# Optimization experiments

Hardware: AMD Instinct MI355X
Metric: run time of the kernel (lower is better)

Reference implementation:

```python
import jax, jax.numpy as jnp
import numpy as np

N = 50000      # nodes
E = 800000     # edges (avg degree 16)
LM = 1024      # lm_dim
H = 128        # hidden_channels
OUT = 64       # out_channels


def setup_inputs() -> dict:
    key = jax.random.key(0)
    ks = jax.random.split(key, 13)
    s = 0.02
    return {
        "x": jax.random.normal(ks[0], (N,), dtype=jnp.float32),
        "x_out": jax.random.normal(ks[1], (N, LM), dtype=jnp.float32),
        "c": jax.random.normal(ks[2], (N,), dtype=jnp.float32),
        "edge_index": jax.random.randint(ks[3], (2, E), 0, N, dtype=jnp.int64),
        "edge_weight": jax.random.uniform(ks[4], (E,), dtype=jnp.float32),
        # weights stored as [in, out]
        "Wa": jax.random.normal(ks[5], (1, LM), dtype=jnp.float32) * s,   # aa_linear (no bias)
        "Wc": jax.random.normal(ks[6], (1, LM), dtype=jnp.float32) * s,   # c_linear (no bias)
        "Wl": jax.random.normal(ks[7], (LM, LM), dtype=jnp.float32) * s,  # lm_linear
        "bl": jax.random.normal(ks[8], (LM,), dtype=jnp.float32) * s,
        "W1": jax.random.normal(ks[9], (LM, H), dtype=jnp.float32) * s,   # conv1
        "b1": jax.random.normal(ks[10], (H,), dtype=jnp.float32) * s,
        "W3": jax.random.normal(ks[11], (H, OUT), dtype=jnp.float32) * s,  # conv3
        "b3": jax.random.normal(ks[12], (OUT,), dtype=jnp.float32) * s,
    }


def gcn_conv(h, src, dst, ew, W, b, n):
    """PyG GCNConv with normalize=True, add_self_loops=True."""
    h = h @ W                                   # [n, out]
    loop = jnp.arange(n, dtype=src.dtype)
    src_f = jnp.concatenate([src, loop])
    dst_f = jnp.concatenate([dst, loop])
    ew_f = jnp.concatenate([ew, jnp.ones((n,), ew.dtype)])
    deg = jax.ops.segment_sum(ew_f, dst_f, num_segments=n)     # in-degree incl. self-loops
    dis = jnp.where(deg > 0, jax.lax.rsqrt(deg), 0.0)          # deg^{-1/2}
    norm = dis[src_f] * ew_f * dis[dst_f]                      # per-edge coefficient
    out = jax.ops.segment_sum(norm[:, None] * h[src_f], dst_f, num_segments=n)
    return out + b


def reference(x, x_out, c, edge_index, edge_weight, Wa, Wc, Wl, bl, W1, b1, W3, b3):
    # (c_linear(c[:,None]) + aa_linear(x[:,None]) + lm_linear(x_out)).relu()
    h = jax.nn.relu(c[:, None] * Wc[0] + x[:, None] * Wa[0] + x_out @ Wl + bl)  # [N, LM]
    src, dst = edge_index[0], edge_index[1]
    h = jax.nn.relu(gcn_conv(h, src, dst, edge_weight, W1, b1, N))              # [N, H]
    return gcn_conv(h, src, dst, edge_weight, W3, b3, N)                        # [N, OUT]
```

## Files before the change

### kernel.cpp

```cpp
#include <hip/hip_runtime.h>
#include <hip/hip_bf16.h>

typedef unsigned short u16;
typedef __attribute__((ext_vector_type(8))) short bf16x8;
typedef __attribute__((ext_vector_type(4))) float f32x4;

constexpr int NN = 50000;
constexpr int NE = 800000;
constexpr int LM = 1024;
constexpr int HC = 128;
constexpr int OC = 64;

constexpr size_t OFF_ROWPTR = 0;
constexpr size_t OFF_CURSOR = 200192;
constexpr size_t OFF_COUNTS = 400384;
constexpr size_t OFF_INCL   = 600576;
constexpr size_t OFF_BSUM   = 800768;
constexpr size_t OFF_BOFF   = 801024;
constexpr size_t OFF_DIS    = 801280;
constexpr size_t OFF_CSRC   = 1001472;
constexpr size_t OFF_CSW    = 4201472;
constexpr size_t OFF_WLT    = 7401472;
constexpr size_t OFF_W1T    = 9498624;
constexpr size_t OFF_H      = 9760768;
constexpr size_t OFF_Y1     = 112160768;
constexpr size_t OFF_H1     = 124960768;
constexpr size_t OFF_Y3     = 137760768;

__device__ __forceinline__ u16 f2bf(float f) {
    union { float f; unsigned int u; } a; a.f = f;
    unsigned int u = a.u + 0x7FFFu + ((a.u >> 16) & 1u);
    return (u16)(u >> 16);
}
__device__ __forceinline__ float bf2f(u16 v) {
    union { unsigned int u; float f; } a; a.u = ((unsigned int)v) << 16;
    return a.f;
}
__device__ __forceinline__ ushort2 pkbf(float a, float b) {
    union { __hip_bfloat162 h; ushort2 u; } cv;
    cv.h = __float22bfloat162_rn(make_float2(a, b));
    return cv.u;
}
__device__ __forceinline__ void async_copy16(u16* lds, const u16* g) {
    __builtin_amdgcn_global_load_lds(
        (const __attribute__((address_space(1))) void*)g,
        (__attribute__((address_space(3))) void*)lds, 16, 0, 0);
}

__global__ void k_zero(int* counts) {
    int i = blockIdx.x * 256 + threadIdx.x;
    if (i < NN) counts[i] = 0;
}
__global__ void k_count(const int* __restrict__ ei, int* __restrict__ counts) {
    int e = blockIdx.x * 256 + threadIdx.x;
    if (e < NE) atomicAdd(&counts[ei[NE + e]], 1);
}
__global__ void k_scan1(const int* __restrict__ counts, int* __restrict__ incl,
                        int* __restrict__ bsum) {
    __shared__ int sm[1024];
    int t = threadIdx.x, idx = blockIdx.x * 1024 + t;
    int v = (idx < NN) ? counts[idx] : 0;
    sm[t] = v; __syncthreads();
    for (int off = 1; off < 1024; off <<= 1) {
        int add = (t >= off) ? sm[t - off] : 0;
        __syncthreads();
        sm[t] += add;
        __syncthreads();
    }
    if (idx < NN) incl[idx] = sm[t];
    if (t == 1023) bsum[blockIdx.x] = sm[t];
}
__global__ void k_scan2(const int* __restrict__ bsum, int* __restrict__ boff, int nb) {
    if (threadIdx.x == 0 && blockIdx.x == 0) {
        int run = 0;
        for (int i = 0; i < nb; i++) { boff[i] = run; run += bsum[i]; }
    }
}
__global__ void k_scan3(const int* __restrict__ incl, const int* __restrict__ counts,
                        const int* __restrict__ boff, int* __restrict__ rowptr,
                        int* __restrict__ cursor) {
    int idx = blockIdx.x * 256 + threadIdx.x;
    if (idx < NN) {
        int rp = incl[idx] - counts[idx] + boff[idx >> 10];
        rowptr[idx] = rp;
        cursor[idx] = rp;
    } else if (idx == NN) {
        rowptr[NN] = NE;
    }
}
__global__ void k_fill(const int* __restrict__ ei, const float* __restrict__ ew,
                       int* __restrict__ cursor, int* __restrict__ csrc,
                       float* __restrict__ csw) {
    int e = blockIdx.x * 256 + threadIdx.x;
    if (e < NE) {
        int d = ei[NE + e];
        int slot = atomicAdd(&cursor[d], 1);
        csrc[slot] = ei[e];
        csw[slot] = ew[e];
    }
}
__global__ void k_deg(const int* __restrict__ rowptr, const float* __restrict__ csw,
                      float* __restrict__ dis) {
    int i = blockIdx.x * 256 + threadIdx.x;
    if (i >= NN) return;
    float d = 1.0f;
    int p1 = rowptr[i + 1];
    for (int p = rowptr[i]; p < p1; ++p) d += csw[p];
    dis[i] = rsqrtf(d);
}
__global__ void k_wnorm(const int* __restrict__ csrc, float* __restrict__ csw,
                        const float* __restrict__ dis) {
    int p = blockIdx.x * 256 + threadIdx.x;
    if (p < NE) csw[p] = csw[p] * dis[csrc[p]];
}

__global__ void k_cvtWl(const float* __restrict__ Wl, u16* __restrict__ WlT) {
    __shared__ float sm[32][33];
    int k0 = blockIdx.y * 32, n0 = blockIdx.x * 32;
    sm[threadIdx.y][threadIdx.x] = Wl[(size_t)(k0 + threadIdx.y) * LM + n0 + threadIdx.x];
    __syncthreads();
    WlT[(size_t)(n0 + threadIdx.y) * LM + k0 + threadIdx.x] = f2bf(sm[threadIdx.x][threadIdx.y]);
}
__global__ void k_cvtW1(const float* __restrict__ W1, u16* __restrict__ W1T) {
    int idx = blockIdx.x * 256 + threadIdx.x;
    if (idx >= HC * LM) return;
    int o = idx >> 10, k = idx & 1023;
    W1T[idx] = f2bf(W1[(size_t)k * HC + o]);
}

template <int MODE>
__global__ __launch_bounds__(256, 2) void k_gemm(
    const void* __restrict__ Aptr, const u16* __restrict__ Bt, u16* __restrict__ Cout,
    int M, int Nn, int K, int nby,
    const float* __restrict__ xv, const float* __restrict__ cv,
    const float* __restrict__ Wa, const float* __restrict__ Wc,
    const float* __restrict__ bl) {
    __shared__ u16 lA[128 * 64];
    __shared__ u16 lB[128 * 64];
    const int tid = threadIdx.x;
    const int lane = tid & 63, wv = tid >> 6;
    const int mtiles = (M + 127) >> 7;
    int bx, by;
    if (nby > 1) {
        int x = blockIdx.x & 7, j = blockIdx.x >> 3;
        bx = (j & ~7) | x;
        by = j & 7;
        if (bx >= mtiles) return;
    } else {
        bx = blockIdx.x; by = 0;
    }
    const int m0 = bx * 128, n0 = by * 128;
    const int wm = (wv >> 1) * 64, wn = (wv & 1) * 64;
    const int fr = lane & 15, qd = lane >> 4;
    const int nt = K >> 6;

    f32x4 acc[4][4] = {};
    const float* A32 = (const float*)Aptr;

    int srl[4], sslot[4]; const float* sbase[4];
    float4 pf[8];
    if constexpr (MODE == 1) {
        #pragma unroll
        for (int i = 0; i < 4; i++) {
            int cidx = i * 256 + tid;
            srl[i] = cidx >> 3; sslot[i] = cidx & 7;
            int k8 = sslot[i] ^ (srl[i] & 7);
            int row = m0 + srl[i]; if (row >= M) row = M - 1;
            sbase[i] = A32 + (size_t)row * K + k8 * 8;
        }
        #pragma unroll
        for (int i = 0; i < 4; i++) {
            pf[2 * i]     = *(const float4*)(sbase[i]);
            pf[2 * i + 1] = *(const float4*)(sbase[i] + 4);
        }
    }

    for (int kt = 0; kt < nt; kt++) {
        const int k0 = kt << 6;
        __syncthreads();
        #pragma unroll
        for (int i = 0; i < 4; i++) {
            int r0 = i * 32 + wv * 8;
            int rl = r0 + (lane >> 3);
            int slot = lane & 7;
            int k8 = slot ^ (rl & 7);
            int col = n0 + rl; if (col >= Nn) col = Nn - 1;
            const u16* g = Bt + (size_t)col * K + k0 + k8 * 8;
            async_copy16(&lB[r0 * 64], g);
        }
        if constexpr (MODE == 2) {
            #pragma unroll
            for (int i = 0; i < 4; i++) {
                int r0 = i * 32 + wv * 8;
                int rl = r0 + (lane >> 3);
                int slot = lane & 7;
                int k8 = slot ^ (rl & 7);
                int row = m0 + rl; if (row >= M) row = M - 1;
                const u16* g = (const u16*)Aptr + (size_t)row * K + k0 + k8 * 8;
                async_copy16(&lA[r0 * 64], g);
            }
        } else {
            #pragma unroll
            for (int i = 0; i < 4; i++) {
                union { ushort2 u2[4]; bf16x8 v; } pk;
                pk.u2[0] = pkbf(pf[2 * i].x, pf[2 * i].y);
                pk.u2[1] = pkbf(pf[2 * i].z, pf[2 * i].w);
                pk.u2[2] = pkbf(pf[2 * i + 1].x, pf[2 * i + 1].y);
                pk.u2[3] = pkbf(pf[2 * i + 1].z, pf[2 * i + 1].w);
                *(bf16x8*)&lA[srl[i] * 64 + sslot[i] * 8] = pk.v;
            }
        }
        __syncthreads();
        if constexpr (MODE == 1) {
            if (kt + 1 < nt) {
                #pragma unroll
                for (int i = 0; i < 4; i++) {
                    pf[2 * i]     = *(const float4*)(sbase[i] + k0 + 64);
                    pf[2 * i + 1] = *(const float4*)(sbase[i] + k0 + 68);
                }
            }
        }
        #pragma unroll
        for (int s = 0; s < 2; s++) {
            const int slot = (s * 4 + qd) ^ (fr & 7);
            bf16x8 af[4], bfm[4];
            #pragma unroll
            for (int mi = 0; mi < 4; mi++)
                af[mi] = *(const bf16x8*)&lA[(wm + mi * 16 + fr) * 64 + slot * 8];
            #pragma unroll
            for (int ni = 0; ni < 4; ni++)
                bfm[ni] = *(const bf16x8*)&lB[(wn + ni * 16 + fr) * 64 + slot * 8];
            #pragma unroll
            for (int mi = 0; mi < 4; mi++)
                #pragma unroll
                for (int ni = 0; ni < 4; ni++)
                    acc[mi][ni] = __builtin_amdgcn_mfma_f32_16x16x32_bf16(
                        af[mi], bfm[ni], acc[mi][ni], 0, 0, 0);
        }
    }

    int jj[4]; float waj[4], wcj[4], blj[4];
    #pragma unroll
    for (int ni = 0; ni < 4; ni++) {
        jj[ni] = n0 + wn + ni * 16 + fr;
        if constexpr (MODE == 1) { waj[ni] = Wa[jj[ni]]; wcj[ni] = Wc[jj[ni]]; blj[ni] = bl[jj[ni]]; }
    }
    #pragma unroll
    for (int mi = 0; mi < 4; mi++) {
        #pragma unroll
        for (int r = 0; r < 4; r++) {
            int row = m0 + wm + mi * 16 + qd * 4 + r;
            if (row < M) {
                float xb = 0.f, cb = 0.f;
                if constexpr (MODE == 1) { xb = xv[row]; cb = cv[row]; }
                #pragma unroll
                for (int ni = 0; ni < 4; ni++) {
                    float v = acc[mi][ni][r];
                    if constexpr (MODE == 1) {
                        v += xb * waj[ni] + cb * wcj[ni] + blj[ni];
                        v = fmaxf(v, 0.f);
                    }
                    Cout[(size_t)row * Nn + jj[ni]] = f2bf(v);
                }
            }
        }
    }
}

__global__ __launch_bounds__(256) void k_agg1(
    const u16* __restrict__ y1, const int* __restrict__ rowptr,
    const int* __restrict__ csrc, const float* __restrict__ csw,
    const float* __restrict__ dis, const float* __restrict__ b1,
    u16* __restrict__ h1) {
    int node = blockIdx.x * 4 + (threadIdx.x >> 6);
    int lane = threadIdx.x & 63;
    if (node >= NN) return;
    float di = dis[node];
    int p0 = rowptr[node], p1 = rowptr[node + 1];
    ushort2 sv = *(const ushort2*)(y1 + (size_t)node * HC + lane * 2);
    float a0 = di * bf2f(sv.x), a1 = di * bf2f(sv.y);
    #pragma unroll 4
    for (int p = p0; p < p1; ++p) {
        int s = csrc[p];
        float nm = csw[p];
        ushort2 v = *(const ushort2*)(y1 + (size_t)s * HC + lane * 2);
        a0 += nm * bf2f(v.x);
        a1 += nm * bf2f(v.y);
    }
    a0 = fmaxf(di * a0 + b1[lane * 2], 0.f);
    a1 = fmaxf(di * a1 + b1[lane * 2 + 1], 0.f);
    ushort2 r; r.x = f2bf(a0); r.y = f2bf(a1);
    *(ushort2*)(h1 + (size_t)node * HC + lane * 2) = r;
}

__global__ __launch_bounds__(256) void k_gemm3(
    const u16* __restrict__ h1, const float* __restrict__ W3, u16* __restrict__ y3) {
    int node = blockIdx.x * 4 + (threadIdx.x >> 6);
    int o = threadIdx.x & 63;
    if (node >= NN) return;
    const u16* hrow = h1 + (size_t)node * HC;
    float acc = 0.f;
    #pragma unroll 16
    for (int k = 0; k < HC; ++k)
        acc += bf2f(hrow[k]) * W3[(size_t)k * OC + o];
    y3[(size_t)node * OC + o] = f2bf(acc);
}

__global__ __launch_bounds__(256) void k_agg3(
    const u16* __restrict__ y3, const int* __restrict__ rowptr,
    const int* __restrict__ csrc, const float* __restrict__ csw,
    const float* __restrict__ dis, const float* __restrict__ b3,
    float* __restrict__ outp) {
    int node = blockIdx.x * 4 + (threadIdx.x >> 6);
    int lane = threadIdx.x & 63;
    if (node >= NN) return;
    float di = dis[node];
    int p0 = rowptr[node], p1 = rowptr[node + 1];
    float a = di * bf2f(y3[(size_t)node * OC + lane]);
    #pragma unroll 4
    for (int p = p0; p < p1; ++p) {
        int s = csrc[p];
        a += csw[p] * bf2f(y3[(size_t)s * OC + lane]);
    }
    outp[(size_t)node * OC + lane] = di * a + b3[lane];
}

extern "C" void kernel_launch(void* const* d_in, const int* in_sizes, int n_in,
                              void* d_out, int out_size, void* d_ws, size_t ws_size,
                              hipStream_t stream) {
    const float* x    = (const float*)d_in[0];
    const float* xout = (const float*)d_in[1];
    const float* c    = (const float*)d_in[2];
    const int*   ei   = (const int*)d_in[3];
    const float* ew   = (const float*)d_in[4];
    const float* Wa   = (const float*)d_in[5];
    const float* Wc   = (const float*)d_in[6];
    const float* Wl   = (const float*)d_in[7];
    const float* bl   = (const float*)d_in[8];
    const float* W1   = (const float*)d_in[9];
    const float* b1   = (const float*)d_in[10];
    const float* W3   = (const float*)d_in[11];
    const float* b3   = (const float*)d_in[12];
    float* outp = (float*)d_out;

    char* ws = (char*)d_ws;
    int*   rowptr = (int*)(ws + OFF_ROWPTR);
    int*   cursor = (int*)(ws + OFF_CURSOR);
    int*   counts = (int*)(ws + OFF_COUNTS);
    int*   incl   = (int*)(ws + OFF_INCL);
    int*   bsum   = (int*)(ws + OFF_BSUM);
    int*   boff   = (int*)(ws + OFF_BOFF);
    float* dis    = (float*)(ws + OFF_DIS);
    int*   csrc   = (int*)(ws + OFF_CSRC);
    float* csw    = (float*)(ws + OFF_CSW);
    u16*   WlT    = (u16*)(ws + OFF_WLT);
    u16*   W1T    = (u16*)(ws + OFF_W1T);
    u16*   hbuf   = (u16*)(ws + OFF_H);
    u16*   y1     = (u16*)(ws + OFF_Y1);
    u16*   h1     = (u16*)(ws + OFF_H1);
    u16*   y3     = (u16*)(ws + OFF_Y3);

    k_zero <<<196, 256, 0, stream>>>(counts);
    k_count<<<3125, 256, 0, stream>>>(ei, counts);
    k_scan1<<<49, 1024, 0, stream>>>(counts, incl, bsum);
    k_scan2<<<1, 64, 0, stream>>>(bsum, boff, 49);
    k_scan3<<<196, 256, 0, stream>>>(incl, counts, boff, rowptr, cursor);
    k_fill <<<3125, 256, 0, stream>>>(ei, ew, cursor, csrc, csw);
    k_deg  <<<196, 256, 0, stream>>>(rowptr, csw, dis);
    k_wnorm<<<3125, 256, 0, stream>>>(csrc, csw, dis);

    k_cvtWl<<<dim3(32, 32), dim3(32, 32), 0, stream>>>(Wl, WlT);
    k_cvtW1<<<512, 256, 0, stream>>>(W1, W1T);

    k_gemm<1><<<392 * 8, 256, 0, stream>>>(xout, WlT, hbuf, NN, LM, LM, 8,
                                           x, c, Wa, Wc, bl);
    k_gemm<2><<<391, 256, 0, stream>>>(hbuf, W1T, y1, NN, HC, LM, 1,
                                       nullptr, nullptr, nullptr, nullptr, nullptr);
    k_agg1<<<12500, 256, 0, stream>>>(y1, rowptr, csrc, csw, dis, b1, h1);
    k_gemm3<<<12500, 256, 0, stream>>>(h1, W3, y3);
    k_agg3<<<12500, 256, 0, stream>>>(y3, rowptr, csrc, csw, dis, b3, outp);
}
```

Measured before the change: 720.3 us.

## Fuse agg1 with gemm3, pack CSR metadata, compute degree via atomics

Merges the zeroing and weight-conversion kernels into one setup launch. Degree is now accumulated with float atomics during edge counting, which removes the separate degree pass. Source index and edge weight are packed into one int2 array so aggregation reads one 8-byte load per edge. The first aggregation is fused with the 128x64 projection through per-wave shared memory, which removes the h1 round trip and one launch; the in-wave LDS handoff relies on wave-synchronous execution.

```diff
diff --git a/kernel.cpp b/kernel.cpp
--- a/kernel.cpp
+++ b/kernel.cpp
@@ -18,13 +18,12 @@
 constexpr size_t OFF_BSUM   = 800768;
 constexpr size_t OFF_BOFF   = 801024;
 constexpr size_t OFF_DIS    = 801280;
-constexpr size_t OFF_CSRC   = 1001472;
-constexpr size_t OFF_CSW    = 4201472;
+constexpr size_t OFF_META   = 1001472;
 constexpr size_t OFF_WLT    = 7401472;
 constexpr size_t OFF_W1T    = 9498624;
 constexpr size_t OFF_H      = 9760768;
 constexpr size_t OFF_Y1     = 112160768;
-constexpr size_t OFF_H1     = 124960768;
+constexpr size_t OFF_DEGF   = 124960768;
 constexpr size_t OFF_Y3     = 137760768;
 
 __device__ __forceinline__ u16 f2bf(float f) {
@@ -47,13 +46,42 @@
         (__attribute__((address_space(3))) void*)lds, 16, 0, 0);
 }
 
-__global__ void k_zero(int* counts) {
-    int i = blockIdx.x * 256 + threadIdx.x;
-    if (i < NN) counts[i] = 0;
-}
-__global__ void k_count(const int* __restrict__ ei, int* __restrict__ counts) {
+__global__ void k_setup(int* __restrict__ counts, float* __restrict__ degf,
+                        const float* __restrict__ Wl, u16* __restrict__ WlT,
+                        const float* __restrict__ W1, u16* __restrict__ W1T) {
+    int b = blockIdx.x, t = threadIdx.x;
+    if (b < 196) {
+        int i = b * 256 + t;
+        if (i < NN) { counts[i] = 0; degf[i] = 0.f; }
+    } else if (b < 196 + 1024) {
+        __shared__ float sm[32][33];
+        int bb = b - 196;
+        int n0 = (bb & 31) * 32, k0 = (bb >> 5) * 32;
+        int ty = t >> 5, tx = t & 31;
+        #pragma unroll
+        for (int i = 0; i < 4; i++)
+            sm[ty + i * 8][tx] = Wl[(size_t)(k0 + ty + i * 8) * LM + n0 + tx];
+        __syncthreads();
+        #pragma unroll
+        for (int i = 0; i < 4; i++)
+            WlT[(size_t)(n0 + ty + i * 8) * LM + k0 + tx] = f2bf(sm[tx][ty + i * 8]);
+    } else {
+        int idx = (b - 1220) * 256 + t;
+        if (idx < HC * LM) {
+            int o = idx >> 10, k = idx & 1023;
+            W1T[idx] = f2bf(W1[(size_t)k * HC + o]);
+        }
+    }
+}
+
+__global__ void k_count(const int* __restrict__ ei, const float* __restrict__ ew,
+                        int* __restrict__ counts, float* __restrict__ degf) {
     int e = blockIdx.x * 256 + threadIdx.x;
-    if (e < NE) atomicAdd(&counts[ei[NE + e]], 1);
+    if (e < NE) {
+        int d = ei[NE + e];
+        atomicAdd(&counts[d], 1);
+        atomicAdd(&degf[d], ew[e]);
+    }
 }
 __global__ void k_scan1(const int* __restrict__ counts, int* __restrict__ incl,
                         int* __restrict__ bsum) {
@@ -77,55 +105,34 @@
     }
 }
 __global__ void k_scan3(const int* __restrict__ incl, const int* __restrict__ counts,
-                        const int* __restrict__ boff, int* __restrict__ rowptr,
-                        int* __restrict__ cursor) {
+                        const int* __restrict__ boff, const float* __restrict__ degf,
+                        int* __restrict__ rowptr, int* __restrict__ cursor,
+                        float* __restrict__ dis) {
     int idx = blockIdx.x * 256 + threadIdx.x;
     if (idx < NN) {
         int rp = incl[idx] - counts[idx] + boff[idx >> 10];
         rowptr[idx] = rp;
         cursor[idx] = rp;
+        dis[idx] = rsqrtf(1.0f + degf[idx]);
     } else if (idx == NN) {
         rowptr[NN] = NE;
     }
 }
 __global__ void k_fill(const int* __restrict__ ei, const float* __restrict__ ew,
-                       int* __restrict__ cursor, int* __restrict__ csrc,
-                       float* __restrict__ csw) {
+                       int* __restrict__ cursor, int2* __restrict__ meta) {
     int e = blockIdx.x * 256 + threadIdx.x;
     if (e < NE) {
         int d = ei[NE + e];
         int slot = atomicAdd(&cursor[d], 1);
-        csrc[slot] = ei[e];
-        csw[slot] = ew[e];
-    }
-}
-__global__ void k_deg(const int* __restrict__ rowptr, const float* __restrict__ csw,
-                      float* __restrict__ dis) {
-    int i = blockIdx.x * 256 + threadIdx.x;
-    if (i >= NN) return;
-    float d = 1.0f;
-    int p1 = rowptr[i + 1];
-    for (int p = rowptr[i]; p < p1; ++p) d += csw[p];
-    dis[i] = rsqrtf(d);
-}
-__global__ void k_wnorm(const int* __restrict__ csrc, float* __restrict__ csw,
-                        const float* __restrict__ dis) {
+        meta[slot] = make_int2(ei[e], __float_as_int(ew[e]));
+    }
+}
+__global__ void k_wnorm(int2* __restrict__ meta, const float* __restrict__ dis) {
     int p = blockIdx.x * 256 + threadIdx.x;
-    if (p < NE) csw[p] = csw[p] * dis[csrc[p]];
-}
-
-__global__ void k_cvtWl(const float* __restrict__ Wl, u16* __restrict__ WlT) {
-    __shared__ float sm[32][33];
-    int k0 = blockIdx.y * 32, n0 = blockIdx.x * 32;
-    sm[threadIdx.y][threadIdx.x] = Wl[(size_t)(k0 + threadIdx.y) * LM + n0 + threadIdx.x];
-    __syncthreads();
-    WlT[(size_t)(n0 + threadIdx.y) * LM + k0 + threadIdx.x] = f2bf(sm[threadIdx.x][threadIdx.y]);
-}
-__global__ void k_cvtW1(const float* __restrict__ W1, u16* __restrict__ W1T) {
-    int idx = blockIdx.x * 256 + threadIdx.x;
-    if (idx >= HC * LM) return;
-    int o = idx >> 10, k = idx & 1023;
-    W1T[idx] = f2bf(W1[(size_t)k * HC + o]);
+    if (p < NE) {
+        int2 m = meta[p];
+        meta[p].y = __float_as_int(__int_as_float(m.y) * dis[m.x]);
+    }
 }
 
 template <int MODE>
@@ -267,60 +274,52 @@
     }
 }
 
-__global__ __launch_bounds__(256) void k_agg1(
+__global__ __launch_bounds__(512) void k_agg1g3(
     const u16* __restrict__ y1, const int* __restrict__ rowptr,
-    const int* __restrict__ csrc, const float* __restrict__ csw,
-    const float* __restrict__ dis, const float* __restrict__ b1,
-    u16* __restrict__ h1) {
-    int node = blockIdx.x * 4 + (threadIdx.x >> 6);
-    int lane = threadIdx.x & 63;
+    const int2* __restrict__ meta, const float* __restrict__ dis,
+    const float* __restrict__ b1, const float* __restrict__ W3,
+    u16* __restrict__ y3) {
+    __shared__ float hrow[8][HC];
+    int wv = threadIdx.x >> 6, lane = threadIdx.x & 63;
+    int node = blockIdx.x * 8 + wv;
     if (node >= NN) return;
     float di = dis[node];
     int p0 = rowptr[node], p1 = rowptr[node + 1];
     ushort2 sv = *(const ushort2*)(y1 + (size_t)node * HC + lane * 2);
     float a0 = di * bf2f(sv.x), a1 = di * bf2f(sv.y);
-    #pragma unroll 4
+    #pragma unroll 8
     for (int p = p0; p < p1; ++p) {
-        int s = csrc[p];
-        float nm = csw[p];
-        ushort2 v = *(const ushort2*)(y1 + (size_t)s * HC + lane * 2);
+        int2 m = meta[p];
+        float nm = __int_as_float(m.y);
+        ushort2 v = *(const ushort2*)(y1 + (size_t)m.x * HC + lane * 2);
         a0 += nm * bf2f(v.x);
         a1 += nm * bf2f(v.y);
     }
     a0 = fmaxf(di * a0 + b1[lane * 2], 0.f);
     a1 = fmaxf(di * a1 + b1[lane * 2 + 1], 0.f);
-    ushort2 r; r.x = f2bf(a0); r.y = f2bf(a1);
-    *(ushort2*)(h1 + (size_t)node * HC + lane * 2) = r;
-}
-
-__global__ __launch_bounds__(256) void k_gemm3(
-    const u16* __restrict__ h1, const float* __restrict__ W3, u16* __restrict__ y3) {
-    int node = blockIdx.x * 4 + (threadIdx.x >> 6);
-    int o = threadIdx.x & 63;
-    if (node >= NN) return;
-    const u16* hrow = h1 + (size_t)node * HC;
+    hrow[wv][lane * 2] = a0;
+    hrow[wv][lane * 2 + 1] = a1;
     float acc = 0.f;
-    #pragma unroll 16
+    #pragma unroll 8
     for (int k = 0; k < HC; ++k)
-        acc += bf2f(hrow[k]) * W3[(size_t)k * OC + o];
-    y3[(size_t)node * OC + o] = f2bf(acc);
+        acc += hrow[wv][k] * W3[(size_t)k * OC + lane];
+    y3[(size_t)node * OC + lane] = f2bf(acc);
 }
 
 __global__ __launch_bounds__(256) void k_agg3(
     const u16* __restrict__ y3, const int* __restrict__ rowptr,
-    const int* __restrict__ csrc, const float* __restrict__ csw,
-    const float* __restrict__ dis, const float* __restrict__ b3,
-    float* __restrict__ outp) {
+    const int2* __restrict__ meta, const float* __restrict__ dis,
+    const float* __restrict__ b3, float* __restrict__ outp) {
     int node = blockIdx.x * 4 + (threadIdx.x >> 6);
     int lane = threadIdx.x & 63;
     if (node >= NN) return;
     float di = dis[node];
     int p0 = rowptr[node], p1 = rowptr[node + 1];
     float a = di * bf2f(y3[(size_t)node * OC + lane]);
-    #pragma unroll 4
+    #pragma unroll 8
     for (int p = p0; p < p1; ++p) {
-        int s = csrc[p];
-        a += csw[p] * bf2f(y3[(size_t)s * OC + lane]);
+        int2 m = meta[p];
+        a += __int_as_float(m.y) * bf2f(y3[(size_t)m.x * OC + lane]);
     }
     outp[(size_t)node * OC + lane] = di * a + b3[lane];
 }
@@ -351,32 +350,26 @@
     int*   bsum   = (int*)(ws + OFF_BSUM);
     int*   boff   = (int*)(ws + OFF_BOFF);
     float* dis    = (float*)(ws + OFF_DIS);
-    int*   csrc   = (int*)(ws + OFF_CSRC);
-    float* csw    = (float*)(ws + OFF_CSW);
+    int2*  meta   = (int2*)(ws + OFF_META);
     u16*   WlT    = (u16*)(ws + OFF_WLT);
     u16*   W1T    = (u16*)(ws + OFF_W1T);
     u16*   hbuf   = (u16*)(ws + OFF_H);
     u16*   y1     = (u16*)(ws + OFF_Y1);
-    u16*   h1     = (u16*)(ws + OFF_H1);
+    float* degf   = (float*)(ws + OFF_DEGF);
     u16*   y3     = (u16*)(ws + OFF_Y3);
 
-    k_zero <<<196, 256, 0, stream>>>(counts);
-    k_count<<<3125, 256, 0, stream>>>(ei, counts);
+    k_setup<<<1732, 256, 0, stream>>>(counts, degf, Wl, WlT, W1, W1T);
+    k_count<<<3125, 256, 0, stream>>>(ei, ew, counts, degf);
     k_scan1<<<49, 1024, 0, stream>>>(counts, incl, bsum);
     k_scan2<<<1, 64, 0, stream>>>(bsum, boff, 49);
-    k_scan3<<<196, 256, 0, stream>>>(incl, counts, boff, rowptr, cursor);
-    k_fill <<<3125, 256, 0, stream>>>(ei, ew, cursor, csrc, csw);
-    k_deg  <<<196, 256, 0, stream>>>(rowptr, csw, dis);
-    k_wnorm<<<3125, 256, 0, stream>>>(csrc, csw, dis);
-
-    k_cvtWl<<<dim3(32, 32), dim3(32, 32), 0, stream>>>(Wl, WlT);
-    k_cvtW1<<<512, 256, 0, stream>>>(W1, W1T);
+    k_scan3<<<196, 256, 0, stream>>>(incl, counts, boff, degf, rowptr, cursor, dis);
+    k_fill <<<3125, 256, 0, stream>>>(ei, ew, cursor, meta);
+    k_wnorm<<<3125, 256, 0, stream>>>(meta, dis);
 
     k_gemm<1><<<392 * 8, 256, 0, stream>>>(xout, WlT, hbuf, NN, LM, LM, 8,
                                            x, c, Wa, Wc, bl);
     k_gemm<2><<<391, 256, 0, stream>>>(hbuf, W1T, y1, NN, HC, LM, 1,
                                        nullptr, nullptr, nullptr, nullptr, nullptr);
-    k_agg1<<<12500, 256, 0, stream>>>(y1, rowptr, csrc, csw, dis, b1, h1);
-    k_gemm3<<<12500, 256, 0, stream>>>(h1, W3, y3);
-    k_agg3<<<12500, 256, 0, stream>>>(y3, rowptr, csrc, csw, dis, b3, outp);
-}
+    k_agg1g3<<<6250, 512, 0, stream>>>(y1, rowptr, meta, dis, b1, W3, y3);
+    k_agg3<<<12500, 256, 0, stream>>>(y3, rowptr, meta, dis, b3, outp);
+}
```

Result: no change. 714.3 us (-0.8%).
